# Kernel optimization log

Hardware: AMD Instinct MI355X
Metric: run time of the kernel (lower is better)

## Reference

```python
import jax, jax.numpy as jnp
import numpy as np

B = 131072
D = 64


def _ln(x, s, b):
    m = x.mean(-1, keepdims=True)
    v = ((x - m) ** 2).mean(-1, keepdims=True)
    return (x - m) / jnp.sqrt(v + 1e-5) * s + b


def _channel_attn(x, inw, inb, ow, ob, nh):
    # x: [B, C, L]; queries/keys are the avg-pooled vector expanded over L
    Bx, C, L = x.shape
    dh = C // nh
    xv = jnp.swapaxes(x, 1, 2)                      # [B, L, C]
    pooled = x.mean(axis=2)                         # [B, C]
    wq, wk, wv = jnp.split(inw, 3, axis=0)
    bq, bk, bv = jnp.split(inb, 3, axis=0)
    q = (pooled @ wq.T + bq).reshape(Bx, nh, dh)
    k = (pooled @ wk.T + bk).reshape(Bx, nh, dh)
    v = (xv @ wv.T + bv).reshape(Bx, L, nh, dh)
    # all query/key rows identical -> one score per (batch, head), broadcast to [L, L]
    s = jnp.einsum('bhd,bhd->bh', q, k) / jnp.sqrt(jnp.asarray(dh, x.dtype))
    scores = jnp.broadcast_to(s[:, :, None, None], (Bx, nh, L, L))
    p = jax.nn.softmax(scores, axis=-1)             # uniform 1/L
    o = jnp.einsum('bhij,bjhd->bihd', p, v).reshape(Bx, L, C)
    o = o @ ow.T + ob
    return xv * o                                    # [B, L, C] (weighted values)


def _spatial(xlc, cw, cb, fw, fb):
    # conv2d with kernel == full (C, L) map -> single contraction per out-channel
    h = jnp.einsum('blc,ocl->bo', xlc, cw) + cb      # [B, 32]
    h = jax.nn.elu(h)                                # pool skipped: spatial dims are 1x1
    return h @ fw.T + fb                             # [B, 64]


def reference(eeg, eog, eeg_inw, eeg_inb, eeg_ow, eeg_ob, eog_inw, eog_inb, eog_ow, eog_ob,
              eeg_cw, eeg_cb, eeg_fw, eeg_fb, eog_cw, eog_cb, eog_fw, eog_fb,
              fus_w, fus_b, tl_ln1_s, tl_ln1_b, tl_inw, tl_inb, tl_ow, tl_ob,
              tl_ln2_s, tl_ln2_b, tl_w1, tl_b1, tl_w2, tl_b2, fn_s, fn_b, cls_w, cls_b):
    eeg_w = _channel_attn(eeg, eeg_inw, eeg_inb, eeg_ow, eeg_ob, 2)
    eog_w = _channel_attn(eog, eog_inw, eog_inb, eog_ow, eog_ob, 1)
    ef = _spatial(eeg_w, eeg_cw, eeg_cb, eeg_fw, eeg_fb)
    of = _spatial(eog_w, eog_cw, eog_cb, eog_fw, eog_fb)
    feat = jnp.concatenate([ef, of], axis=-1) @ fus_w.T + fus_b   # [B, 64]
    # positional encoding at position 0: sin(0)=0 on even dims, cos(0)=1 on odd dims
    pe0 = (jnp.arange(D) % 2).astype(feat.dtype)
    feat = feat + pe0
    # 2-layer norm_first transformer encoder on a length-1 sequence
    for i in range(2):
        h = _ln(feat, tl_ln1_s[i], tl_ln1_b[i])
        # seq_len == 1: softmax over one key is exactly 1 (zero grad to q,k scores)
        attn = (h @ tl_inw[i, 2 * D:].T + tl_inb[i, 2 * D:]) @ tl_ow[i].T + tl_ob[i]
        feat = feat + attn
        h2 = _ln(feat, tl_ln2_s[i], tl_ln2_b[i])
        feat = feat + jax.nn.gelu(h2 @ tl_w1[i].T + tl_b1[i], approximate=False) @ tl_w2[i].T + tl_b2[i]
    feat = _ln(feat, fn_s, fn_b)
    return feat @ cls_w.T + cls_b                    # [B, 3]


def setup_inputs() -> dict:
    key = jax.random.key(0)
    it = iter(jax.random.split(key, 40))

    def rn(shape, s=0.1):
        return jax.random.normal(next(it), shape, jnp.float32) * s

    return {
        'eeg': jax.random.normal(next(it), (B, 62, 5), jnp.float32),
        'eog': jax.random.normal(next(it), (B, 1, 33), jnp.float32),
        'eeg_inw': rn((186, 62)), 'eeg_inb': rn((186,)), 'eeg_ow': rn((62, 62)), 'eeg_ob': rn((62,)),
        'eog_inw': rn((3, 1)), 'eog_inb': rn((3,)), 'eog_ow': rn((1, 1)), 'eog_ob': rn((1,)),
        'eeg_cw': rn((32, 62, 5)), 'eeg_cb': rn((32,)), 'eeg_fw': rn((64, 32)), 'eeg_fb': rn((64,)),
        'eog_cw': rn((32, 1, 33)), 'eog_cb': rn((32,)), 'eog_fw': rn((64, 32)), 'eog_fb': rn((64,)),
        'fus_w': rn((64, 128)), 'fus_b': rn((64,)),
        'tl_ln1_s': jnp.ones((2, 64), jnp.float32), 'tl_ln1_b': jnp.zeros((2, 64), jnp.float32),
        'tl_inw': rn((2, 192, 64)), 'tl_inb': rn((2, 192)), 'tl_ow': rn((2, 64, 64)), 'tl_ob': rn((2, 64)),
        'tl_ln2_s': jnp.ones((2, 64), jnp.float32), 'tl_ln2_b': jnp.zeros((2, 64), jnp.float32),
        'tl_w1': rn((2, 256, 64)), 'tl_b1': rn((2, 256)), 'tl_w2': rn((2, 64, 256)), 'tl_b2': rn((2, 64)),
        'fn_s': jnp.ones((64,), jnp.float32), 'fn_b': jnp.zeros((64,), jnp.float32),
        'cls_w': rn((3, 64)), 'cls_b': rn((3,)),
    }
```

## Files before the change

kernel.cpp:

```cpp
#include <hip/hip_runtime.h>
#include <hip/hip_bf16.h>
#include <math.h>

#define NB 131072

typedef __attribute__((ext_vector_type(2))) float f32x2;
typedef __attribute__((ext_vector_type(4))) float f32x4;
typedef __attribute__((ext_vector_type(8))) short bf16x8;
typedef __attribute__((ext_vector_type(4))) short s16x4;

#define SYNC() do { asm volatile("" ::: "memory"); __builtin_amdgcn_sched_barrier(0x7F); } while (0)

#define WS_A_EEG 0
#define WS_A_EOG 2048
#define WS_B0    4096
#define WS_WATT  4160
#define WS_BATT  12352
#define WS_WVT   12480
#define WS_M     16324
#define WS_OBB   20168
#define WS_CWT   20232
#define WS_CWOG  30152
#define WS_W2T   31208
#define WB_WA_F  64000
#define WB_W1_F  68096
#define WB_W2_F  84480
#define WB_MB    100864
#define WB_CWL   102912
#define WB_ACAT  108032
#define WB_CWOG2 110080
#define WB_EEGXB 111104
#define WB_POOLB (WB_EEGXB + 155 * NB)
#define WB_EOGB  (WB_POOLB + 32 * NB)
#define WS_TOTALF (WB_EOGB + 17 * NB)

#define ROWB 208
#define WAVE_LDS (64 * ROWB)

__device__ __forceinline__ short f2bf(float x) {
    union { __hip_bfloat16 h; short s; } u;
    u.h = __float2bfloat16(x);
    return u.s;
}
__device__ __forceinline__ float bf2f(unsigned short s) {
    union { unsigned int u; float f; } v;
    v.u = (unsigned int)s << 16;
    return v.f;
}
__device__ __forceinline__ float gelu_fast(float v) {
    float u = v * v;
    float w = v * fmaf(0.044715f, u, 1.0f);
    float x = fminf(w * 2.302118131f, 80.f);
    float e = __builtin_exp2f(x);
    float t = (e - 1.0f) * __builtin_amdgcn_rcpf(e + 1.0f);
    float hv = 0.5f * v;
    return fmaf(hv, t, hv);
}
__device__ __forceinline__ float elu_f(float x) {
    return x > 0.f ? x : (__builtin_exp2f(x * 1.4426950408889634f) - 1.0f);
}

__global__ __launch_bounds__(256) void mcaf_pre(
    const float* __restrict__ eeg_inw, const float* __restrict__ eeg_inb,
    const float* __restrict__ eeg_ow,  const float* __restrict__ eeg_ob,
    const float* __restrict__ eeg_cw,
    const float* __restrict__ eeg_fw,  const float* __restrict__ eeg_fb,
    const float* __restrict__ eog_cw,  const float* __restrict__ eog_fw,
    const float* __restrict__ eog_fb,
    const float* __restrict__ fus_w,   const float* __restrict__ fus_b,
    const float* __restrict__ tl_inw,  const float* __restrict__ tl_inb,
    const float* __restrict__ tl_ow,   const float* __restrict__ tl_ob,
    const float* __restrict__ tl_w1,   const float* __restrict__ tl_w2,
    float* __restrict__ ws, int full)
{
    const int tid  = blockIdx.x * blockDim.x + threadIdx.x;
    const int nthr = gridDim.x * blockDim.x;
    short* wa_b   = (short*)(ws + WB_WA_F);
    short* w1_b   = (short*)(ws + WB_W1_F);
    short* w2_b   = (short*)(ws + WB_W2_F);
    short* mb_b   = (short*)(ws + WB_MB);
    short* cwl_b  = (short*)(ws + WB_CWL);
    short* acat_b = (short*)(ws + WB_ACAT);
    short* cwog2  = (short*)(ws + WB_CWOG2);

    for (int idx = tid; idx < 4096; idx += nthr) {
        int f = idx >> 6, j = idx & 63;
        float a = 0.f;
        if (j < 32) {
            for (int k = 0; k < 64; ++k)
                a = fmaf(fus_w[f * 128 + k], eeg_fw[k * 32 + j], a);
        } else {
            int o = j - 32;
            for (int k = 0; k < 64; ++k)
                a = fmaf(fus_w[f * 128 + 64 + k], eog_fw[k * 32 + o], a);
        }
        acat_b[idx] = f2bf(a);
    }
    for (int f = tid; f < 64; f += nthr) {
        float a = fus_b[f] + (float)(f & 1);
        for (int k = 0; k < 64; ++k) {
            a = fmaf(fus_w[f * 128 + k],      eeg_fb[k], a);
            a = fmaf(fus_w[f * 128 + 64 + k], eog_fb[k], a);
        }
        ws[WS_B0 + f] = a;
    }
    for (int idx = tid; idx < 8192; idx += nthr) {
        int i = idx >> 12, c = (idx >> 6) & 63, d = idx & 63;
        float a = 0.f;
        for (int e = 0; e < 64; ++e)
            a = fmaf(tl_ow[i * 4096 + c * 64 + e],
                     tl_inw[i * 12288 + (128 + e) * 64 + d], a);
        if (!full) ws[WS_WATT + idx] = a;
        wa_b[idx] = f2bf(a);
    }
    for (int idx = tid; idx < 128; idx += nthr) {
        int i = idx >> 6, c = idx & 63;
        float a = tl_ob[i * 64 + c];
        for (int e = 0; e < 64; ++e)
            a = fmaf(tl_ow[i * 4096 + c * 64 + e], tl_inb[i * 192 + 128 + e], a);
        ws[WS_BATT + idx] = a;
    }
    for (int idx = tid; idx < 32768; idx += nthr) w1_b[idx] = f2bf(tl_w1[idx]);
    for (int idx = tid; idx < 32768; idx += nthr) w2_b[idx] = f2bf(tl_w2[idx]);

    for (int idx = tid; idx < 4096; idx += nthr) {
        int c = idx >> 6, e = idx & 63;
        float a = 0.f;
        if (c < 62) {
            if (e < 62) {
                for (int d = 0; d < 62; ++d)
                    a = fmaf(eeg_ow[c * 62 + d], eeg_inw[(124 + d) * 62 + e], a);
            } else if (e == 62) {
                a = eeg_ob[c];
                for (int d = 0; d < 62; ++d)
                    a = fmaf(eeg_ow[c * 62 + d], eeg_inb[124 + d], a);
            }
        }
        mb_b[idx] = f2bf(a);
    }
    for (int idx = tid; idx < 10240; idx += nthr) {
        int o = idx / 320, k = idx - o * 320;
        int l = k >> 6, c = k & 63;
        float a = (c < 62 && l < 5) ? eeg_cw[o * 310 + c * 5 + l] : 0.f;
        cwl_b[idx] = f2bf(a);
    }
    for (int idx = tid; idx < 2048; idx += nthr) {
        int o = idx >> 6, l = idx & 63;
        cwog2[idx] = f2bf(l < 33 ? eog_cw[o * 33 + l] : 0.f);
    }

    if (!full) {
        for (int idx = tid; idx < 2048; idx += nthr) {
            int f = idx >> 5, o = idx & 31;
            float a = 0.f, a2 = 0.f;
            for (int k = 0; k < 64; ++k) {
                a  = fmaf(fus_w[f * 128 + k],      eeg_fw[k * 32 + o], a);
                a2 = fmaf(fus_w[f * 128 + 64 + k], eog_fw[k * 32 + o], a2);
            }
            ws[WS_A_EEG + idx] = a;
            ws[WS_A_EOG + idx] = a2;
        }
        for (int idx = tid; idx < 3844; idx += nthr) {
            int e = idx / 62, d = idx - e * 62;
            ws[WS_WVT + idx] = eeg_inw[(124 + d) * 62 + e];
        }
        for (int idx = tid; idx < 3844; idx += nthr) {
            int c = idx / 62, e = idx - c * 62;
            float a = 0.f;
            for (int d = 0; d < 62; ++d)
                a = fmaf(eeg_ow[c * 62 + d], eeg_inw[(124 + d) * 62 + e], a);
            ws[WS_M + idx] = a;
        }
        for (int c = tid; c < 62; c += nthr) {
            float a = eeg_ob[c];
            for (int d = 0; d < 62; ++d)
                a = fmaf(eeg_ow[c * 62 + d], eeg_inb[124 + d], a);
            ws[WS_OBB + c] = a;
        }
        for (int idx = tid; idx < 9920; idx += nthr) {
            int c = idx / 160, r = idx - c * 160;
            int o = r / 5, l = r - o * 5;
            ws[WS_CWT + idx] = eeg_cw[o * 310 + c * 5 + l];
        }
        for (int idx = tid; idx < 1056; idx += nthr) {
            int l = idx >> 5, o = idx & 31;
            ws[WS_CWOG + idx] = eog_cw[o * 33 + l];
        }
        for (int idx = tid; idx < 32768; idx += nthr) {
            int i = idx >> 14, r = idx & 16383;
            int j = r >> 6, c = r & 63;
            ws[WS_W2T + idx] = tl_w2[i * 16384 + c * 256 + j];
        }
    }
}

__global__ __launch_bounds__(256) void mcaf_tr(const float* __restrict__ eeg,
                                               const float* __restrict__ eog,
                                               float* __restrict__ ws)
{
    __shared__ short smem[4 * 64 * 42];
    const int lane = threadIdx.x & 63;
    const int wid  = threadIdx.x >> 6;
    const int nEeg = (NB / 256) * 8;

    if ((int)blockIdx.x < nEeg) {
        const int chunk = blockIdx.x & 7;
        const int bw    = ((int)blockIdx.x >> 3) * 256 + wid * 64;
        const int b     = bw + lane;
        short* sw = smem + wid * (64 * 42);

        const int ch0 = chunk * 40;
        for (int j = 0; j < 20; ++j) {
            int idx = j * 64 + lane;
            int r = idx / 20, cc2 = idx - r * 20;
            int gcol = ch0 + cc2 * 2;
            unsigned int pack = 0;
            if (gcol < 310) {
                f32x2 v = *(const f32x2*)(eeg + (size_t)(bw + r) * 310 + gcol);
                pack = (unsigned int)(unsigned short)f2bf(v[0]) |
                       ((unsigned int)(unsigned short)f2bf(v[1]) << 16);
            }
            *(unsigned int*)(sw + r * 42 + cc2 * 2) = pack;
        }
        SYNC();
        const short* myrow = sw + lane * 42;
        unsigned int* planes = (unsigned int*)(ws + WB_EEGXB);
        #pragma unroll
        for (int pr = 0; pr < 4; ++pr) {
            int c0 = chunk * 8 + pr * 2;
            if (c0 < 62) {
                int cp = c0 >> 1;
                #pragma unroll
                for (int l = 0; l < 5; ++l) {
                    unsigned int d = (unsigned int)(unsigned short)myrow[pr * 10 + l] |
                                     ((unsigned int)(unsigned short)myrow[pr * 10 + 5 + l] << 16);
                    planes[(size_t)(l * 31 + cp) * NB + b] = d;
                }
            }
        }
        bf16x8 pv;
        #pragma unroll
        for (int el = 0; el < 8; ++el) {
            int c = chunk * 8 + el;
            float p;
            if (c < 62) {
                float s = bf2f((unsigned short)myrow[el * 5 + 0]);
                s += bf2f((unsigned short)myrow[el * 5 + 1]);
                s += bf2f((unsigned short)myrow[el * 5 + 2]);
                s += bf2f((unsigned short)myrow[el * 5 + 3]);
                s += bf2f((unsigned short)myrow[el * 5 + 4]);
                p = s * 0.2f;
            } else {
                p = (c == 62) ? 1.0f : 0.f;
            }
            pv[el] = f2bf(p);
        }
        *(bf16x8*)((short*)(ws + WB_POOLB) + ((size_t)chunk * NB + b) * 8) = pv;
    } else {
        const int bid = (int)blockIdx.x - nEeg;
        const int bw  = bid * 256 + wid * 64;
        float* swf = (float*)smem + wid * (64 * 34);

        for (int j = 0; j < 33; ++j) {
            int idx = j * 64 + lane;
            int r = idx / 33, cc = idx - r * 33;
            swf[r * 34 + cc] = eog[(size_t)(bw + r) * 33 + cc];
        }
        SYNC();
        unsigned int* EOGB = (unsigned int*)(ws + WB_EOGB);
        const float* xr = swf + lane * 34;
        #pragma unroll
        for (int cp = 0; cp < 16; ++cp) {
            unsigned int d = (unsigned int)(unsigned short)f2bf(xr[2 * cp]) |
                             ((unsigned int)(unsigned short)f2bf(xr[2 * cp + 1]) << 16);
            EOGB[(size_t)cp * NB + bw + lane] = d;
        }
        EOGB[(size_t)16 * NB + bw + lane] = (unsigned int)(unsigned short)f2bf(xr[32]);
    }
}

__global__ __launch_bounds__(256, 2) void mcaf_fused(
    const float* __restrict__ eeg_cb,
    const float* __restrict__ eog_inw, const float* __restrict__ eog_inb,
    const float* __restrict__ eog_ow,  const float* __restrict__ eog_ob,
    const float* __restrict__ eog_cb,
    const float* __restrict__ tl_ln1_s, const float* __restrict__ tl_ln1_b,
    const float* __restrict__ tl_ln2_s, const float* __restrict__ tl_ln2_b,
    const float* __restrict__ tl_b1,   const float* __restrict__ tl_b2,
    const float* __restrict__ fn_s,    const float* __restrict__ fn_b,
    const float* __restrict__ cls_w,   const float* __restrict__ cls_b,
    const float* __restrict__ ws,      float* __restrict__ out)
{
    __shared__ char smem[4 * WAVE_LDS];
    const int tid  = threadIdx.x;
    const int lane = tid & 63;
    const int wid  = tid >> 6;
    const int b    = blockIdx.x * 256 + tid;
    char* Wv = smem + wid * WAVE_LDS;
    const int g4  = lane >> 4;
    const int r15 = lane & 15;

    const short* MB    = (const short*)(ws + WB_MB);
    const short* CWL   = (const short*)(ws + WB_CWL);
    const short* ACAT  = (const short*)(ws + WB_ACAT);
    const short* CWOG2 = (const short*)(ws + WB_CWOG2);
    const short* PB    = (const short*)(ws + WB_POOLB);
    const unsigned int* XP = (const unsigned int*)(ws + WB_EEGXB);

    #pragma unroll
    for (int q = 0; q < 8; ++q) {
        bf16x8 v = *(const bf16x8*)(PB + ((size_t)q * NB + b) * 8);
        *(bf16x8*)(Wv + lane * ROWB + q * 16) = v;
    }
    SYNC();
    bf16x8 Ap[4][2];
    #pragma unroll
    for (int rt = 0; rt < 4; ++rt)
        #pragma unroll
        for (int kt = 0; kt < 2; ++kt)
            Ap[rt][kt] = *(const bf16x8*)(Wv + (rt * 16 + r15) * ROWB + (kt * 4 + g4) * 16);
    SYNC();
    f32x4 accO[4][4];
    #pragma unroll
    for (int ct = 0; ct < 4; ++ct)
        #pragma unroll
        for (int rt = 0; rt < 4; ++rt) accO[ct][rt] = (f32x4){0.f, 0.f, 0.f, 0.f};
    __builtin_amdgcn_s_setprio(1);
    #pragma unroll
    for (int kt = 0; kt < 2; ++kt) {
        bf16x8 bb[4];
        #pragma unroll
        for (int ct = 0; ct < 4; ++ct)
            bb[ct] = *(const bf16x8*)(MB + (ct * 16 + r15) * 64 + kt * 32 + g4 * 8);
        #pragma unroll
        for (int ct = 0; ct < 4; ++ct)
            #pragma unroll
            for (int rt = 0; rt < 4; ++rt)
                accO[ct][rt] = __builtin_amdgcn_mfma_f32_16x16x32_bf16(bb[ct], Ap[rt][kt], accO[ct][rt], 0, 0, 0);
    }
    __builtin_amdgcn_s_setprio(0);
    float oc[64];
    #pragma unroll
    for (int hf = 0; hf < 2; ++hf) {
        SYNC();
        #pragma unroll
        for (int ct2 = 0; ct2 < 2; ++ct2)
            #pragma unroll
            for (int rt = 0; rt < 4; ++rt)
                *(f32x4*)(Wv + (rt * 16 + r15) * ROWB + (ct2 * 16 + g4 * 4) * 4) = accO[hf * 2 + ct2][rt];
        SYNC();
        #pragma unroll
        for (int j8 = 0; j8 < 8; ++j8) {
            f32x4 v = *(const f32x4*)(Wv + lane * ROWB + j8 * 16);
            #pragma unroll
            for (int e = 0; e < 4; ++e) oc[hf * 32 + j8 * 4 + e] = v[e];
        }
    }

    f32x4 accH[2][4];
    #pragma unroll
    for (int ct = 0; ct < 2; ++ct)
        #pragma unroll
        for (int rt = 0; rt < 4; ++rt) accH[ct][rt] = (f32x4){0.f, 0.f, 0.f, 0.f};
    for (int l = 0; l < 5; ++l) {
        SYNC();
        #pragma unroll
        for (int jj = 0; jj < 8; ++jj) {
            bf16x8 v;
            #pragma unroll
            for (int q = 0; q < 4; ++q) {
                int cp = jj * 4 + q;
                if (cp < 31) {
                    unsigned int d = XP[(size_t)(l * 31 + cp) * NB + b];
                    v[2 * q]     = f2bf(oc[2 * cp]     * bf2f((unsigned short)(d & 0xffffu)));
                    v[2 * q + 1] = f2bf(oc[2 * cp + 1] * bf2f((unsigned short)(d >> 16)));
                } else {
                    v[2 * q] = 0; v[2 * q + 1] = 0;
                }
            }
            *(bf16x8*)(Wv + lane * ROWB + jj * 16) = v;
        }
        SYNC();
        bf16x8 a[4][2];
        #pragma unroll
        for (int rt = 0; rt < 4; ++rt)
            #pragma unroll
            for (int kt = 0; kt < 2; ++kt)
                a[rt][kt] = *(const bf16x8*)(Wv + (rt * 16 + r15) * ROWB + (kt * 4 + g4) * 16);
        SYNC();
        __builtin_amdgcn_s_setprio(1);
        #pragma unroll
        for (int kt = 0; kt < 2; ++kt) {
            bf16x8 bb[2];
            #pragma unroll
            for (int ct = 0; ct < 2; ++ct)
                bb[ct] = *(const bf16x8*)(CWL + (ct * 16 + r15) * 320 + l * 64 + kt * 32 + g4 * 8);
            #pragma unroll
            for (int ct = 0; ct < 2; ++ct)
                #pragma unroll
                for (int rt = 0; rt < 4; ++rt)
                    accH[ct][rt] = __builtin_amdgcn_mfma_f32_16x16x32_bf16(bb[ct], a[rt][kt], accH[ct][rt], 0, 0, 0);
        }
        __builtin_amdgcn_s_setprio(0);
    }
    float h[32];
    SYNC();
    #pragma unroll
    for (int ct2 = 0; ct2 < 2; ++ct2)
        #pragma unroll
        for (int rt = 0; rt < 4; ++rt)
            *(f32x4*)(Wv + (rt * 16 + r15) * ROWB + (ct2 * 16 + g4 * 4) * 4) = accH[ct2][rt];
    SYNC();
    #pragma unroll
    for (int j8 = 0; j8 < 8; ++j8) {
        f32x4 v = *(const f32x4*)(Wv + lane * ROWB + j8 * 16);
        #pragma unroll
        for (int e = 0; e < 4; ++e) h[j8 * 4 + e] = v[e] + eeg_cb[j8 * 4 + e];
    }
    #pragma unroll
    for (int o = 0; o < 32; ++o) h[o] = elu_f(h[o]);

    float Tg[32];
    {
        const unsigned int* EOGB = (const unsigned int*)(ws + WB_EOGB);
        unsigned int ed[17];
        #pragma unroll
        for (int cp = 0; cp < 17; ++cp) ed[cp] = EOGB[(size_t)cp * NB + b];
        float pool = 0.f;
        #pragma unroll
        for (int cp = 0; cp < 16; ++cp) {
            pool += bf2f((unsigned short)(ed[cp] & 0xffffu));
            pool += bf2f((unsigned short)(ed[cp] >> 16));
        }
        pool += bf2f((unsigned short)(ed[16] & 0xffffu));
        SYNC();
        #pragma unroll
        for (int jj = 0; jj < 8; ++jj) {
            union { unsigned int u[4]; bf16x8 v; } pk;
            if (jj < 4) {
                pk.u[0] = ed[4 * jj]; pk.u[1] = ed[4 * jj + 1];
                pk.u[2] = ed[4 * jj + 2]; pk.u[3] = ed[4 * jj + 3];
            } else if (jj == 4) {
                pk.u[0] = ed[16]; pk.u[1] = 0; pk.u[2] = 0; pk.u[3] = 0;
            } else {
                pk.u[0] = 0; pk.u[1] = 0; pk.u[2] = 0; pk.u[3] = 0;
            }
            *(bf16x8*)(Wv + lane * ROWB + jj * 16) = pk.v;
        }
        SYNC();
        bf16x8 a[4][2];
        #pragma unroll
        for (int rt = 0; rt < 4; ++rt)
            #pragma unroll
            for (int kt = 0; kt < 2; ++kt)
                a[rt][kt] = *(const bf16x8*)(Wv + (rt * 16 + r15) * ROWB + (kt * 4 + g4) * 16);
        SYNC();
        f32x4 accE[2][4];
        #pragma unroll
        for (int ct = 0; ct < 2; ++ct)
            #pragma unroll
            for (int rt = 0; rt < 4; ++rt) accE[ct][rt] = (f32x4){0.f, 0.f, 0.f, 0.f};
        __builtin_amdgcn_s_setprio(1);
        #pragma unroll
        for (int kt = 0; kt < 2; ++kt) {
            bf16x8 bb[2];
            #pragma unroll
            for (int ct = 0; ct < 2; ++ct)
                bb[ct] = *(const bf16x8*)(CWOG2 + (ct * 16 + r15) * 64 + kt * 32 + g4 * 8);
            #pragma unroll
            for (int ct = 0; ct < 2; ++ct)
                #pragma unroll
                for (int rt = 0; rt < 4; ++rt)
                    accE[ct][rt] = __builtin_amdgcn_mfma_f32_16x16x32_bf16(bb[ct], a[rt][kt], accE[ct][rt], 0, 0, 0);
        }
        __builtin_amdgcn_s_setprio(0);
        SYNC();
        #pragma unroll
        for (int ct2 = 0; ct2 < 2; ++ct2)
            #pragma unroll
            for (int rt = 0; rt < 4; ++rt)
                *(f32x4*)(Wv + (rt * 16 + r15) * ROWB + (ct2 * 16 + g4 * 4) * 4) = accE[ct2][rt];
        SYNC();
        float tp[32];
        #pragma unroll
        for (int j8 = 0; j8 < 8; ++j8) {
            f32x4 v = *(const f32x4*)(Wv + lane * ROWB + j8 * 16);
            #pragma unroll
            for (int e = 0; e < 4; ++e) tp[j8 * 4 + e] = v[e];
        }
        pool *= (1.f / 33.f);
        float vb2 = fmaf(pool, eog_inw[2], eog_inb[2]);
        float ob2 = fmaf(vb2, eog_ow[0], eog_ob[0]);
        #pragma unroll
        for (int o = 0; o < 32; ++o)
            Tg[o] = elu_f(fmaf(ob2, tp[o], eog_cb[o]));
    }

    SYNC();
    #pragma unroll
    for (int jj = 0; jj < 8; ++jj) {
        bf16x8 v;
        #pragma unroll
        for (int e = 0; e < 8; ++e) {
            int j = jj * 8 + e;
            v[e] = f2bf(j < 32 ? h[j] : Tg[j - 32]);
        }
        *(bf16x8*)(Wv + lane * ROWB + jj * 16) = v;
    }
    SYNC();
    bf16x8 Ac[4][2];
    #pragma unroll
    for (int rt = 0; rt < 4; ++rt)
        #pragma unroll
        for (int kt = 0; kt < 2; ++kt)
            Ac[rt][kt] = *(const bf16x8*)(Wv + (rt * 16 + r15) * ROWB + (kt * 4 + g4) * 16);
    SYNC();
    f32x4 accF[4][4];
    #pragma unroll
    for (int ct = 0; ct < 4; ++ct)
        #pragma unroll
        for (int rt = 0; rt < 4; ++rt) accF[ct][rt] = (f32x4){0.f, 0.f, 0.f, 0.f};
    __builtin_amdgcn_s_setprio(1);
    #pragma unroll
    for (int kt = 0; kt < 2; ++kt) {
        bf16x8 bb[4];
        #pragma unroll
        for (int ct = 0; ct < 4; ++ct)
            bb[ct] = *(const bf16x8*)(ACAT + (ct * 16 + r15) * 64 + kt * 32 + g4 * 8);
        #pragma unroll
        for (int ct = 0; ct < 4; ++ct)
            #pragma unroll
            for (int rt = 0; rt < 4; ++rt)
                accF[ct][rt] = __builtin_amdgcn_mfma_f32_16x16x32_bf16(bb[ct], Ac[rt][kt], accF[ct][rt], 0, 0, 0);
    }
    __builtin_amdgcn_s_setprio(0);
    float feat[64];
    #pragma unroll
    for (int hf = 0; hf < 2; ++hf) {
        SYNC();
        #pragma unroll
        for (int ct2 = 0; ct2 < 2; ++ct2)
            #pragma unroll
            for (int rt = 0; rt < 4; ++rt)
                *(f32x4*)(Wv + (rt * 16 + r15) * ROWB + (ct2 * 16 + g4 * 4) * 4) = accF[hf * 2 + ct2][rt];
        SYNC();
        #pragma unroll
        for (int j8 = 0; j8 < 8; ++j8) {
            f32x4 v = *(const f32x4*)(Wv + lane * ROWB + j8 * 16);
            #pragma unroll
            for (int e = 0; e < 4; ++e) {
                int d = hf * 32 + j8 * 4 + e;
                feat[d] = v[e] + ws[WS_B0 + d];
            }
        }
    }

    const short* WAb = (const short*)(ws + WB_WA_F);
    const short* W1b = (const short*)(ws + WB_W1_F);
    const short* W2b = (const short*)(ws + WB_W2_F);

    for (int i2 = 0; i2 < 2; ++i2) {
        const float* ba  = ws + WS_BATT + i2 * 64;
        const float* s1  = tl_ln1_s + i2 * 64;
        const float* gb1 = tl_ln1_b + i2 * 64;
        const float* s2  = tl_ln2_s + i2 * 64;
        const float* gb2 = tl_ln2_b + i2 * 64;
        const float* bf1 = tl_b1 + i2 * 256;
        const float* bf2 = tl_b2 + i2 * 64;

        float hb[64];
        {
            float m = 0.f;
            #pragma unroll
            for (int d = 0; d < 64; ++d) m += feat[d];
            m *= 0.015625f;
            float vv = 0.f;
            #pragma unroll
            for (int d = 0; d < 64; ++d) { float u = feat[d] - m; vv = fmaf(u, u, vv); }
            vv *= 0.015625f;
            float inv = rsqrtf(vv + 1e-5f);
// ... 301 lines not shown
            pool += x;
            const float* cr = ws + WS_CWOG + l2 * 32;
            #pragma unroll
            for (int o = 0; o < 32; ++o) Tg[o] = fmaf(x, cr[o], Tg[o]);
        }
        pool *= (1.f / 33.f);
        float vb2 = fmaf(pool, eog_inw[2], eog_inb[2]);
        float ob2 = fmaf(vb2, eog_ow[0], eog_ob[0]);
        #pragma unroll
        for (int o = 0; o < 32; ++o) {
            float hh = fmaf(ob2, Tg[o], eog_cb[o]);
            Tg[o] = hh > 0.f ? hh : expm1f(hh);
        }
        #pragma unroll
        for (int f = 0; f < 64; ++f) {
            float acc = feat[f];
            #pragma unroll
            for (int o = 0; o < 32; ++o)
                acc = fmaf(ws[WS_A_EOG + f * 32 + o], Tg[o], acc);
            feat[f] = acc;
        }
    }

    for (int i2 = 0; i2 < 2; ++i2) {
        const float* Wa  = ws + WS_WATT + i2 * 4096;
        const float* ba  = ws + WS_BATT + i2 * 64;
        const float* s1  = tl_ln1_s + i2 * 64;
        const float* g1  = tl_ln1_b + i2 * 64;
        const float* s2  = tl_ln2_s + i2 * 64;
        const float* g2  = tl_ln2_b + i2 * 64;
        const float* w1p = tl_w1 + i2 * 16384;
        const float* bf1 = tl_b1 + i2 * 256;
        const float* w2t = ws + WS_W2T + i2 * 16384;
        const float* bf2 = tl_b2 + i2 * 64;

        float hb[64];
        {
            float m = 0.f;
            #pragma unroll
            for (int d = 0; d < 64; ++d) m += feat[d];
            m *= 0.015625f;
            float vv = 0.f;
            #pragma unroll
            for (int d = 0; d < 64; ++d) { float u = feat[d] - m; vv = fmaf(u, u, vv); }
            vv *= 0.015625f;
            float inv = rsqrtf(vv + 1e-5f);
            #pragma unroll
            for (int d = 0; d < 64; ++d)
                hb[d] = fmaf((feat[d] - m) * inv, s1[d], g1[d]);
        }
        #pragma unroll
        for (int c = 0; c < 64; ++c) {
            float a = ba[c];
            #pragma unroll
            for (int d = 0; d < 64; ++d) a = fmaf(Wa[c * 64 + d], hb[d], a);
            feat[c] += a;
        }
        {
            float m = 0.f;
            #pragma unroll
            for (int d = 0; d < 64; ++d) m += feat[d];
            m *= 0.015625f;
            float vv = 0.f;
            #pragma unroll
            for (int d = 0; d < 64; ++d) { float u = feat[d] - m; vv = fmaf(u, u, vv); }
            vv *= 0.015625f;
            float inv = rsqrtf(vv + 1e-5f);
            #pragma unroll
            for (int d = 0; d < 64; ++d)
                hb[d] = fmaf((feat[d] - m) * inv, s2[d], g2[d]);
        }
        #pragma unroll
        for (int c = 0; c < 64; ++c) feat[c] += bf2[c];
        for (int j = 0; j < 256; ++j) {
            const float* wr = w1p + j * 64;
            float g = bf1[j];
            #pragma unroll
            for (int d = 0; d < 64; ++d) g = fmaf(wr[d], hb[d], g);
            g = 0.5f * g * (1.f + erff(g * 0.70710678118654752f));
            const float* w2r = w2t + j * 64;
            #pragma unroll
            for (int c = 0; c < 64; ++c) feat[c] = fmaf(g, w2r[c], feat[c]);
        }
    }

    {
        float m = 0.f;
        #pragma unroll
        for (int d = 0; d < 64; ++d) m += feat[d];
        m *= 0.015625f;
        float vv = 0.f;
        #pragma unroll
        for (int d = 0; d < 64; ++d) { float u = feat[d] - m; vv = fmaf(u, u, vv); }
        vv *= 0.015625f;
        float inv = rsqrtf(vv + 1e-5f);
        float o0 = cls_b[0], o1 = cls_b[1], o2 = cls_b[2];
        #pragma unroll
        for (int d = 0; d < 64; ++d) {
            float n = fmaf((feat[d] - m) * inv, fn_s[d], fn_b[d]);
            o0 = fmaf(n, cls_w[d], o0);
            o1 = fmaf(n, cls_w[64 + d], o1);
            o2 = fmaf(n, cls_w[128 + d], o2);
        }
        float* op = out + b * 3;
        op[0] = o0; op[1] = o1; op[2] = o2;
    }
}

extern "C" void kernel_launch(void* const* d_in, const int* in_sizes, int n_in,
                              void* d_out, int out_size, void* d_ws, size_t ws_size,
                              hipStream_t stream) {
    const float* eeg      = (const float*)d_in[0];
    const float* eog      = (const float*)d_in[1];
    const float* eeg_inw  = (const float*)d_in[2];
    const float* eeg_inb  = (const float*)d_in[3];
    const float* eeg_ow   = (const float*)d_in[4];
    const float* eeg_ob   = (const float*)d_in[5];
    const float* eog_inw  = (const float*)d_in[6];
    const float* eog_inb  = (const float*)d_in[7];
    const float* eog_ow   = (const float*)d_in[8];
    const float* eog_ob   = (const float*)d_in[9];
    const float* eeg_cw   = (const float*)d_in[10];
    const float* eeg_cb   = (const float*)d_in[11];
    const float* eeg_fw   = (const float*)d_in[12];
    const float* eeg_fb   = (const float*)d_in[13];
    const float* eog_cw   = (const float*)d_in[14];
    const float* eog_cb   = (const float*)d_in[15];
    const float* eog_fw   = (const float*)d_in[16];
    const float* eog_fb   = (const float*)d_in[17];
    const float* fus_w    = (const float*)d_in[18];
    const float* fus_b    = (const float*)d_in[19];
    const float* tl_ln1_s = (const float*)d_in[20];
    const float* tl_ln1_b = (const float*)d_in[21];
    const float* tl_inw   = (const float*)d_in[22];
    const float* tl_inb   = (const float*)d_in[23];
    const float* tl_ow    = (const float*)d_in[24];
    const float* tl_ob    = (const float*)d_in[25];
    const float* tl_ln2_s = (const float*)d_in[26];
    const float* tl_ln2_b = (const float*)d_in[27];
    const float* tl_w1    = (const float*)d_in[28];
    const float* tl_b1    = (const float*)d_in[29];
    const float* tl_w2    = (const float*)d_in[30];
    const float* tl_b2    = (const float*)d_in[31];
    const float* fn_s     = (const float*)d_in[32];
    const float* fn_b     = (const float*)d_in[33];
    const float* cls_w    = (const float*)d_in[34];
    const float* cls_b    = (const float*)d_in[35];
    float* ws  = (float*)d_ws;
    float* out = (float*)d_out;

    const size_t need = (size_t)WS_TOTALF * 4u;
    const int full = (ws_size >= need) ? 1 : 0;

    hipLaunchKernelGGL(mcaf_pre, dim3(64), dim3(256), 0, stream,
                       eeg_inw, eeg_inb, eeg_ow, eeg_ob, eeg_cw,
                       eeg_fw, eeg_fb, eog_cw, eog_fw, eog_fb,
                       fus_w, fus_b, tl_inw, tl_inb, tl_ow, tl_ob, tl_w1, tl_w2,
                       ws, full);

    if (full) {
        hipLaunchKernelGGL(mcaf_tr, dim3((NB / 256) * 8 + NB / 256), dim3(256), 0, stream,
                           eeg, eog, ws);
        hipLaunchKernelGGL(mcaf_fused, dim3(NB / 256), dim3(256), 0, stream,
                           eeg_cb, eog_inw, eog_inb, eog_ow, eog_ob, eog_cb,
                           tl_ln1_s, tl_ln1_b, tl_ln2_s, tl_ln2_b,
                           tl_b1, tl_b2, fn_s, fn_b, cls_w, cls_b, ws, out);
    } else {
        hipLaunchKernelGGL(mcaf_main_fb, dim3(NB / 256), dim3(256), 0, stream,
                           eeg, eog, eeg_inb, eeg_ow, eeg_ob,
                           eog_inw, eog_inb, eog_ow, eog_ob,
                           eeg_cb, eog_cb,
                           tl_ln1_s, tl_ln1_b, tl_ln2_s, tl_ln2_b,
                           tl_w1, tl_b1, tl_b2,
                           fn_s, fn_b, cls_w, cls_b, ws, out);
    }
}
```

Before: 197.1 us.

## Merge weight prep into transpose kernel and prefetch activation loads in fused kernel

Measured after the change: 167.2 us. 1.18x faster.

```diff
diff --git a/kernel.cpp b/kernel.cpp
--- a/kernel.cpp
+++ b/kernel.cpp
@@ -60,6 +60,138 @@
     return x > 0.f ? x : (__builtin_exp2f(x * 1.4426950408889634f) - 1.0f);
 }
 
+__device__ void pre_body(
+    const float* __restrict__ eeg_inw, const float* __restrict__ eeg_inb,
+    const float* __restrict__ eeg_ow,  const float* __restrict__ eeg_ob,
+    const float* __restrict__ eeg_cw,
+    const float* __restrict__ eeg_fw,  const float* __restrict__ eeg_fb,
+    const float* __restrict__ eog_cw,  const float* __restrict__ eog_fw,
+    const float* __restrict__ eog_fb,
+    const float* __restrict__ fus_w,   const float* __restrict__ fus_b,
+    const float* __restrict__ tl_inw,  const float* __restrict__ tl_inb,
+    const float* __restrict__ tl_ow,   const float* __restrict__ tl_ob,
+    const float* __restrict__ tl_w1,   const float* __restrict__ tl_w2,
+    float* __restrict__ ws, int full, int tid, int nthr)
+{
+    short* wa_b   = (short*)(ws + WB_WA_F);
+    short* w1_b   = (short*)(ws + WB_W1_F);
+    short* w2_b   = (short*)(ws + WB_W2_F);
+    short* mb_b   = (short*)(ws + WB_MB);
+    short* cwl_b  = (short*)(ws + WB_CWL);
+    short* acat_b = (short*)(ws + WB_ACAT);
+    short* cwog2  = (short*)(ws + WB_CWOG2);
+
+    for (int idx = tid; idx < 4096; idx += nthr) {
+        int f = idx >> 6, j = idx & 63;
+        float a = 0.f;
+        if (j < 32) {
+            for (int k = 0; k < 64; ++k)
+                a = fmaf(fus_w[f * 128 + k], eeg_fw[k * 32 + j], a);
+        } else {
+            int o = j - 32;
+            for (int k = 0; k < 64; ++k)
+                a = fmaf(fus_w[f * 128 + 64 + k], eog_fw[k * 32 + o], a);
+        }
+        acat_b[idx] = f2bf(a);
+    }
+    for (int f = tid; f < 64; f += nthr) {
+        float a = fus_b[f] + (float)(f & 1);
+        for (int k = 0; k < 64; ++k) {
+            a = fmaf(fus_w[f * 128 + k],      eeg_fb[k], a);
+            a = fmaf(fus_w[f * 128 + 64 + k], eog_fb[k], a);
+        }
+        ws[WS_B0 + f] = a;
+    }
+    for (int idx = tid; idx < 8192; idx += nthr) {
+        int i = idx >> 12, c = (idx >> 6) & 63, d = idx & 63;
+        float a = 0.f;
+        for (int e = 0; e < 64; ++e)
+            a = fmaf(tl_ow[i * 4096 + c * 64 + e],
+                     tl_inw[i * 12288 + (128 + e) * 64 + d], a);
+        if (!full) ws[WS_WATT + idx] = a;
+        wa_b[idx] = f2bf(a);
+    }
+    for (int idx = tid; idx < 128; idx += nthr) {
+        int i = idx >> 6, c = idx & 63;
+        float a = tl_ob[i * 64 + c];
+        for (int e = 0; e < 64; ++e)
+            a = fmaf(tl_ow[i * 4096 + c * 64 + e], tl_inb[i * 192 + 128 + e], a);
+        ws[WS_BATT + idx] = a;
+    }
+    for (int idx = tid; idx < 32768; idx += nthr) w1_b[idx] = f2bf(tl_w1[idx]);
+    for (int idx = tid; idx < 32768; idx += nthr) w2_b[idx] = f2bf(tl_w2[idx]);
+
+    for (int idx = tid; idx < 4096; idx += nthr) {
+        int c = idx >> 6, e = idx & 63;
+        float a = 0.f;
+        if (c < 62) {
+            if (e < 62) {
+                for (int d = 0; d < 62; ++d)
+                    a = fmaf(eeg_ow[c * 62 + d], eeg_inw[(124 + d) * 62 + e], a);
+            } else if (e == 62) {
+                a = eeg_ob[c];
+                for (int d = 0; d < 62; ++d)
+                    a = fmaf(eeg_ow[c * 62 + d], eeg_inb[124 + d], a);
+            }
+        }
+        mb_b[idx] = f2bf(a);
+    }
+    for (int idx = tid; idx < 10240; idx += nthr) {
+        int o = idx / 320, k = idx - o * 320;
+        int l = k >> 6, c = k & 63;
+        float a = (c < 62 && l < 5) ? eeg_cw[o * 310 + c * 5 + l] : 0.f;
+        cwl_b[idx] = f2bf(a);
+    }
+    for (int idx = tid; idx < 2048; idx += nthr) {
+        int o = idx >> 6, l = idx & 63;
+        cwog2[idx] = f2bf(l < 33 ? eog_cw[o * 33 + l] : 0.f);
+    }
+
+    if (!full) {
+        for (int idx = tid; idx < 2048; idx += nthr) {
+            int f = idx >> 5, o = idx & 31;
+            float a = 0.f, a2 = 0.f;
+            for (int k = 0; k < 64; ++k) {
+                a  = fmaf(fus_w[f * 128 + k],      eeg_fw[k * 32 + o], a);
+                a2 = fmaf(fus_w[f * 128 + 64 + k], eog_fw[k * 32 + o], a2);
+            }
+            ws[WS_A_EEG + idx] = a;
+            ws[WS_A_EOG + idx] = a2;
+        }
+        for (int idx = tid; idx < 3844; idx += nthr) {
+            int e = idx / 62, d = idx - e * 62;
+            ws[WS_WVT + idx] = eeg_inw[(124 + d) * 62 + e];
+        }
+        for (int idx = tid; idx < 3844; idx += nthr) {
+            int c = idx / 62, e = idx - c * 62;
+            float a = 0.f;
+            for (int d = 0; d < 62; ++d)
+                a = fmaf(eeg_ow[c * 62 + d], eeg_inw[(124 + d) * 62 + e], a);
+            ws[WS_M + idx] = a;
+        }
+        for (int c = tid; c < 62; c += nthr) {
+            float a = eeg_ob[c];
+            for (int d = 0; d < 62; ++d)
+                a = fmaf(eeg_ow[c * 62 + d], eeg_inb[124 + d], a);
+            ws[WS_OBB + c] = a;
+        }
+        for (int idx = tid; idx < 9920; idx += nthr) {
+            int c = idx / 160, r = idx - c * 160;
+            int o = r / 5, l = r - o * 5;
+            ws[WS_CWT + idx] = eeg_cw[o * 310 + c * 5 + l];
+        }
+        for (int idx = tid; idx < 1056; idx += nthr) {
+            int l = idx >> 5, o = idx & 31;
+            ws[WS_CWOG + idx] = eog_cw[o * 33 + l];
+        }
+        for (int idx = tid; idx < 32768; idx += nthr) {
+            int i = idx >> 14, r = idx & 16383;
+            int j = r >> 6, c = r & 63;
+            ws[WS_W2T + idx] = tl_w2[i * 16384 + c * 256 + j];
+        }
+    }
+}
+
 __global__ __launch_bounds__(256) void mcaf_pre(
     const float* __restrict__ eeg_inw, const float* __restrict__ eeg_inb,
     const float* __restrict__ eeg_ow,  const float* __restrict__ eeg_ob,
@@ -73,139 +205,44 @@
     const float* __restrict__ tl_w1,   const float* __restrict__ tl_w2,
     float* __restrict__ ws, int full)
 {
-    const int tid  = blockIdx.x * blockDim.x + threadIdx.x;
-    const int nthr = gridDim.x * blockDim.x;
-    short* wa_b   = (short*)(ws + WB_WA_F);
-    short* w1_b   = (short*)(ws + WB_W1_F);
-    short* w2_b   = (short*)(ws + WB_W2_F);
-    short* mb_b   = (short*)(ws + WB_MB);
-    short* cwl_b  = (short*)(ws + WB_CWL);
-    short* acat_b = (short*)(ws + WB_ACAT);
-    short* cwog2  = (short*)(ws + WB_CWOG2);
-
-    for (int idx = tid; idx < 4096; idx += nthr) {
-        int f = idx >> 6, j = idx & 63;
-        float a = 0.f;
-        if (j < 32) {
-            for (int k = 0; k < 64; ++k)
-                a = fmaf(fus_w[f * 128 + k], eeg_fw[k * 32 + j], a);
-        } else {
-            int o = j - 32;
-            for (int k = 0; k < 64; ++k)
-                a = fmaf(fus_w[f * 128 + 64 + k], eog_fw[k * 32 + o], a);
-        }
-        acat_b[idx] = f2bf(a);
-    }
-    for (int f = tid; f < 64; f += nthr) {
-        float a = fus_b[f] + (float)(f & 1);
-        for (int k = 0; k < 64; ++k) {
-            a = fmaf(fus_w[f * 128 + k],      eeg_fb[k], a);
-            a = fmaf(fus_w[f * 128 + 64 + k], eog_fb[k], a);
-        }
-        ws[WS_B0 + f] = a;
-    }
-    for (int idx = tid; idx < 8192; idx += nthr) {
-        int i = idx >> 12, c = (idx >> 6) & 63, d = idx & 63;
-        float a = 0.f;
-        for (int e = 0; e < 64; ++e)
-            a = fmaf(tl_ow[i * 4096 + c * 64 + e],
-                     tl_inw[i * 12288 + (128 + e) * 64 + d], a);
-        if (!full) ws[WS_WATT + idx] = a;
-        wa_b[idx] = f2bf(a);
-    }
-    for (int idx = tid; idx < 128; idx += nthr) {
-        int i = idx >> 6, c = idx & 63;
-        float a = tl_ob[i * 64 + c];
-        for (int e = 0; e < 64; ++e)
-            a = fmaf(tl_ow[i * 4096 + c * 64 + e], tl_inb[i * 192 + 128 + e], a);
-        ws[WS_BATT + idx] = a;
-    }
-    for (int idx = tid; idx < 32768; idx += nthr) w1_b[idx] = f2bf(tl_w1[idx]);
-    for (int idx = tid; idx < 32768; idx += nthr) w2_b[idx] = f2bf(tl_w2[idx]);
-
-    for (int idx = tid; idx < 4096; idx += nthr) {
-        int c = idx >> 6, e = idx & 63;
-        float a = 0.f;
-        if (c < 62) {
-            if (e < 62) {
-                for (int d = 0; d < 62; ++d)
-                    a = fmaf(eeg_ow[c * 62 + d], eeg_inw[(124 + d) * 62 + e], a);
-            } else if (e == 62) {
-                a = eeg_ob[c];
-                for (int d = 0; d < 62; ++d)
-                    a = fmaf(eeg_ow[c * 62 + d], eeg_inb[124 + d], a);
-            }
-        }
-        mb_b[idx] = f2bf(a);
-    }
-    for (int idx = tid; idx < 10240; idx += nthr) {
-        int o = idx / 320, k = idx - o * 320;
-        int l = k >> 6, c = k & 63;
-        float a = (c < 62 && l < 5) ? eeg_cw[o * 310 + c * 5 + l] : 0.f;
-        cwl_b[idx] = f2bf(a);
-    }
-    for (int idx = tid; idx < 2048; idx += nthr) {
-        int o = idx >> 6, l = idx & 63;
-        cwog2[idx] = f2bf(l < 33 ? eog_cw[o * 33 + l] : 0.f);
-    }
-
-    if (!full) {
-        for (int idx = tid; idx < 2048; idx += nthr) {
-            int f = idx >> 5, o = idx & 31;
-            float a = 0.f, a2 = 0.f;
-            for (int k = 0; k < 64; ++k) {
-                a  = fmaf(fus_w[f * 128 + k],      eeg_fw[k * 32 + o], a);
-                a2 = fmaf(fus_w[f * 128 + 64 + k], eog_fw[k * 32 + o], a2);
-            }
-            ws[WS_A_EEG + idx] = a;
-            ws[WS_A_EOG + idx] = a2;
-        }
-        for (int idx = tid; idx < 3844; idx += nthr) {
-            int e = idx / 62, d = idx - e * 62;
-            ws[WS_WVT + idx] = eeg_inw[(124 + d) * 62 + e];
-        }
-        for (int idx = tid; idx < 3844; idx += nthr) {
-            int c = idx / 62, e = idx - c * 62;
-            float a = 0.f;
-            for (int d = 0; d < 62; ++d)
-                a = fmaf(eeg_ow[c * 62 + d], eeg_inw[(124 + d) * 62 + e], a);
-            ws[WS_M + idx] = a;
-        }
-        for (int c = tid; c < 62; c += nthr) {
-            float a = eeg_ob[c];
-            for (int d = 0; d < 62; ++d)
-                a = fmaf(eeg_ow[c * 62 + d], eeg_inb[124 + d], a);
-            ws[WS_OBB + c] = a;
-        }
-        for (int idx = tid; idx < 9920; idx += nthr) {
-            int c = idx / 160, r = idx - c * 160;
-            int o = r / 5, l = r - o * 5;
-            ws[WS_CWT + idx] = eeg_cw[o * 310 + c * 5 + l];
-        }
-        for (int idx = tid; idx < 1056; idx += nthr) {
-            int l = idx >> 5, o = idx & 31;
-            ws[WS_CWOG + idx] = eog_cw[o * 33 + l];
-        }
-        for (int idx = tid; idx < 32768; idx += nthr) {
-            int i = idx >> 14, r = idx & 16383;
-            int j = r >> 6, c = r & 63;
-            ws[WS_W2T + idx] = tl_w2[i * 16384 + c * 256 + j];
-        }
-    }
+    pre_body(eeg_inw, eeg_inb, eeg_ow, eeg_ob, eeg_cw, eeg_fw, eeg_fb,
+             eog_cw, eog_fw, eog_fb, fus_w, fus_b, tl_inw, tl_inb,
+             tl_ow, tl_ob, tl_w1, tl_w2, ws, full,
+             blockIdx.x * blockDim.x + threadIdx.x, gridDim.x * blockDim.x);
 }
 
-__global__ __launch_bounds__(256) void mcaf_tr(const float* __restrict__ eeg,
-                                               const float* __restrict__ eog,
-                                               float* __restrict__ ws)
+#define PREP_PRE   64
+#define PREP_EEG   ((NB / 256) * 8)
+#define PREP_EOG   (NB / 256)
+__global__ __launch_bounds__(256) void mcaf_prep(
+    const float* __restrict__ eeg,     const float* __restrict__ eog,
+    const float* __restrict__ eeg_inw, const float* __restrict__ eeg_inb,
+    const float* __restrict__ eeg_ow,  const float* __restrict__ eeg_ob,
+    const float* __restrict__ eeg_cw,
+    const float* __restrict__ eeg_fw,  const float* __restrict__ eeg_fb,
+    const float* __restrict__ eog_cw,  const float* __restrict__ eog_fw,
+    const float* __restrict__ eog_fb,
+    const float* __restrict__ fus_w,   const float* __restrict__ fus_b,
+    const float* __restrict__ tl_inw,  const float* __restrict__ tl_inb,
+    const float* __restrict__ tl_ow,   const float* __restrict__ tl_ob,
+    const float* __restrict__ tl_w1,   const float* __restrict__ tl_w2,
+    float* __restrict__ ws)
 {
     __shared__ short smem[4 * 64 * 42];
     const int lane = threadIdx.x & 63;
     const int wid  = threadIdx.x >> 6;
-    const int nEeg = (NB / 256) * 8;
-
-    if ((int)blockIdx.x < nEeg) {
-        const int chunk = blockIdx.x & 7;
-        const int bw    = ((int)blockIdx.x >> 3) * 256 + wid * 64;
+
+    if ((int)blockIdx.x < PREP_PRE) {
+        pre_body(eeg_inw, eeg_inb, eeg_ow, eeg_ob, eeg_cw, eeg_fw, eeg_fb,
+                 eog_cw, eog_fw, eog_fb, fus_w, fus_b, tl_inw, tl_inb,
+                 tl_ow, tl_ob, tl_w1, tl_w2, ws, 1,
+                 blockIdx.x * 256 + threadIdx.x, PREP_PRE * 256);
+        return;
+    }
+    if ((int)blockIdx.x < PREP_PRE + PREP_EEG) {
+        const int bid   = (int)blockIdx.x - PREP_PRE;
+        const int chunk = bid & 7;
+        const int bw    = (bid >> 3) * 256 + wid * 64;
         const int b     = bw + lane;
         short* sw = smem + wid * (64 * 42);
 
@@ -257,7 +294,7 @@
         }
         *(bf16x8*)((short*)(ws + WB_POOLB) + ((size_t)chunk * NB + b) * 8) = pv;
     } else {
-        const int bid = (int)blockIdx.x - nEeg;
+        const int bid = (int)blockIdx.x - PREP_PRE - PREP_EEG;
         const int bw  = bid * 256 + wid * 64;
         float* swf = (float*)smem + wid * (64 * 34);
 
@@ -307,6 +344,13 @@
     const short* PB    = (const short*)(ws + WB_POOLB);
     const unsigned int* XP = (const unsigned int*)(ws + WB_EEGXB);
 
+    unsigned int ed[17];
+    {
+        const unsigned int* EOGB = (const unsigned int*)(ws + WB_EOGB);
+        #pragma unroll
+        for (int cp = 0; cp < 17; ++cp) ed[cp] = EOGB[(size_t)cp * NB + b];
+    }
+
     #pragma unroll
     for (int q = 0; q < 8; ++q) {
         bf16x8 v = *(const bf16x8*)(PB + ((size_t)q * NB + b) * 8);
@@ -362,7 +406,15 @@
     for (int ct = 0; ct < 2; ++ct)
         #pragma unroll
         for (int rt = 0; rt < 4; ++rt) accH[ct][rt] = (f32x4){0.f, 0.f, 0.f, 0.f};
+    unsigned int xp[31], xpn[31];
+    #pragma unroll
+    for (int cp = 0; cp < 31; ++cp) xp[cp] = XP[(size_t)cp * NB + b];
     for (int l = 0; l < 5; ++l) {
+        if (l < 4) {
+            #pragma unroll
+            for (int cp = 0; cp < 31; ++cp)
+                xpn[cp] = XP[(size_t)((l + 1) * 31 + cp) * NB + b];
+        }
         SYNC();
         #pragma unroll
         for (int jj = 0; jj < 8; ++jj) {
@@ -371,7 +423,7 @@
             for (int q = 0; q < 4; ++q) {
                 int cp = jj * 4 + q;
                 if (cp < 31) {
-                    unsigned int d = XP[(size_t)(l * 31 + cp) * NB + b];
+                    unsigned int d = xp[cp];
                     v[2 * q]     = f2bf(oc[2 * cp]     * bf2f((unsigned short)(d & 0xffffu)));
                     v[2 * q + 1] = f2bf(oc[2 * cp + 1] * bf2f((unsigned short)(d >> 16)));
                 } else {
@@ -402,6 +454,8 @@
                     accH[ct][rt] = __builtin_amdgcn_mfma_f32_16x16x32_bf16(bb[ct], a[rt][kt], accH[ct][rt], 0, 0, 0);
         }
         __builtin_amdgcn_s_setprio(0);
+        #pragma unroll
+        for (int cp = 0; cp < 31; ++cp) xp[cp] = xpn[cp];
     }
     float h[32];
     SYNC();
@@ -422,10 +476,6 @@
 
     float Tg[32];
     {
-        const unsigned int* EOGB = (const unsigned int*)(ws + WB_EOGB);
-        unsigned int ed[17];
-        #pragma unroll
-        for (int cp = 0; cp < 17; ++cp) ed[cp] = EOGB[(size_t)cp * NB + b];
         float pool = 0.f;
         #pragma unroll
         for (int cp = 0; cp < 16; ++cp) {
@@ -1033,20 +1083,22 @@
     const size_t need = (size_t)WS_TOTALF * 4u;
     const int full = (ws_size >= need) ? 1 : 0;
 
-    hipLaunchKernelGGL(mcaf_pre, dim3(64), dim3(256), 0, stream,
-                       eeg_inw, eeg_inb, eeg_ow, eeg_ob, eeg_cw,
-                       eeg_fw, eeg_fb, eog_cw, eog_fw, eog_fb,
-                       fus_w, fus_b, tl_inw, tl_inb, tl_ow, tl_ob, tl_w1, tl_w2,
-                       ws, full);
-
     if (full) {
-        hipLaunchKernelGGL(mcaf_tr, dim3((NB / 256) * 8 + NB / 256), dim3(256), 0, stream,
-                           eeg, eog, ws);
+        hipLaunchKernelGGL(mcaf_prep, dim3(PREP_PRE + PREP_EEG + PREP_EOG), dim3(256), 0, stream,
+                           eeg, eog,
+                           eeg_inw, eeg_inb, eeg_ow, eeg_ob, eeg_cw,
+                           eeg_fw, eeg_fb, eog_cw, eog_fw, eog_fb,
+                           fus_w, fus_b, tl_inw, tl_inb, tl_ow, tl_ob, tl_w1, tl_w2, ws);
         hipLaunchKernelGGL(mcaf_fused, dim3(NB / 256), dim3(256), 0, stream,
                            eeg_cb, eog_inw, eog_inb, eog_ow, eog_ob, eog_cb,
                            tl_ln1_s, tl_ln1_b, tl_ln2_s, tl_ln2_b,
                            tl_b1, tl_b2, fn_s, fn_b, cls_w, cls_b, ws, out);
     } else {
+        hipLaunchKernelGGL(mcaf_pre, dim3(64), dim3(256), 0, stream,
+                           eeg_inw, eeg_inb, eeg_ow, eeg_ob, eeg_cw,
+                           eeg_fw, eeg_fb, eog_cw, eog_fw, eog_fb,
+                           fus_w, fus_b, tl_inw, tl_inb, tl_ow, tl_ob, tl_w1, tl_w2,
+                           ws, 0);
         hipLaunchKernelGGL(mcaf_main_fb, dim3(NB / 256), dim3(256), 0, stream,
                            eeg, eog, eeg_inb, eeg_ow, eeg_ob,
                            eog_inw, eog_inb, eog_ow, eog_ob,
```
